# Kernel tuning notes

Measured on AMD Instinct MI355X. Metric: run time of the kernel, lower is better.

Reference implementation:

```python
import jax, jax.numpy as jnp
import numpy as np

ALPHA = 0.2  # LeakyReLU slope
EPS = 1e-5   # LayerNorm eps (torch default)
NEG = -9e15  # pyGAT mask fill


def _lnorm(x, g, b):
    mu = x.mean(-1, keepdims=True)
    var = ((x - mu) ** 2).mean(-1, keepdims=True)
    return (x - mu) / jnp.sqrt(var + EPS) * g + b


def _gat_rel(h, adj, W, a1, a2):
    # Canonical dense GAT layer, vectorized over relations.
    # h [N,di], adj [R,N,N] int, W [R,di,do], a1/a2 [R,do]
    Wh = jnp.einsum('ni,rio->rno', h, W)                     # [R,N,do]
    f1 = jnp.einsum('rno,ro->rn', Wh, a1)
    f2 = jnp.einsum('rno,ro->rn', Wh, a2)
    e = jax.nn.leaky_relu(f1[:, :, None] + f2[:, None, :], ALPHA)  # [R,N,N]
    att = jax.nn.softmax(jnp.where(adj > 0, e, NEG), axis=-1)
    return jax.nn.elu(jnp.einsum('rnm,rmo->rno', att, Wh))   # [R,N,do]


def setup_inputs() -> dict:
    key = jax.random.key(0)
    N, D, R, Q, C = 2048, 512, 4, 32, 64
    HE, HD = 2, 2
    ks = jax.random.split(key, 16)
    s = 0.05
    return {
        'x': jax.random.normal(ks[0], (N, D), jnp.float32),
        'rel_adj': jax.random.randint(ks[1], (R, N, N), 0, 2, jnp.int32),
        'qembedding1': jax.random.normal(ks[2], (Q, D), jnp.float32),
        'qnode_idx': jax.random.randint(ks[3], (8,), 0, N, jnp.int32),
        'choices_nodes_idx': jax.random.randint(ks[4], (5, C), 0, N, jnp.int32),
        'Wc': jax.random.normal(ks[5], (D, D), jnp.float32) * s,
        'bc': jnp.zeros((D,), jnp.float32),
        'wq': jax.random.normal(ks[6], (D,), jnp.float32) * s,
        'enc_W': jax.random.normal(ks[7], (HE, R, D, D), jnp.float32) * s,
        'enc_a1': jax.random.normal(ks[8], (HE, R, D), jnp.float32) * s,
        'enc_a2': jax.random.normal(ks[9], (HE, R, D), jnp.float32) * s,
        'dec_W': jax.random.normal(ks[10], (HD, R, D, D), jnp.float32) * s,
        'dec_a1': jax.random.normal(ks[11], (HD, R, D), jnp.float32) * s,
        'dec_a2': jax.random.normal(ks[12], (HD, R, D), jnp.float32) * s,
        'ln_g': jnp.ones((D,), jnp.float32),
        'ln_b': jnp.zeros((D,), jnp.float32),
        'Wqc': jax.random.normal(ks[13], (D, D), jnp.float32) * s,
        'bqc': jnp.zeros((D,), jnp.float32),
        'Wout': jax.random.normal(ks[14], (D, 1), jnp.float32) * s,
        'bout': jnp.zeros((1,), jnp.float32),
    }


def reference(x, rel_adj, qembedding1, qnode_idx, choices_nodes_idx,
              Wc, bc, wq, enc_W, enc_a1, enc_a2, dec_W, dec_a1, dec_a2,
              ln_g, ln_b, Wqc, bqc, Wout, bout):
    # QuestionLayer: attention-pool the question token sequence -> [D]
    qemb = jax.nn.softmax(qembedding1 @ wq) @ qembedding1
    # question-gated node embeddings (Conv1d k=1 == linear over features)
    p = jax.nn.sigmoid((x @ Wc.T + bc) @ qemb)[:, None]       # [N,1]
    x = p * x + (1.0 - p) * qemb[None, :]
    # encoder: per-relation GAT + LayerNorm, maxpool over relations
    for h in range(enc_W.shape[0]):
        xr = _gat_rel(x, rel_adj, enc_W[h], enc_a1[h], enc_a2[h])
        x = _lnorm(xr, ln_g, ln_b).max(axis=0)                # [N,D]
    # decoder (transpose attentions): last round skips LayerNorm
    xd = x
    HD = dec_W.shape[0]
    for i in range(HD):
        xr = _gat_rel(xd, rel_adj, dec_W[i], dec_a1[i], dec_a2[i])
        if i < HD - 1:
            xr = _lnorm(xr, ln_g, ln_b)
        xd = xr.max(axis=0)
    # QuestionChoiceLayer over the 5 choices (all present -> mask gate = 1)
    cnodes = x[choices_nodes_idx]                             # [5,C,D]
    qproj = qembedding1.mean(axis=0) @ Wqc + bqc              # [D]
    scores = jax.nn.softmax(jnp.einsum('kcd,d->kc', cnodes, qproj), axis=-1)
    cembed = jnp.einsum('kc,kcd->kd', scores, cnodes)         # [5,D]
    cout = jax.nn.log_softmax(cembed @ Wout + bout, axis=0)   # [5,1]
    return cout, xd
```

## Files before the change

kernel.cpp:

```cpp
#include <hip/hip_runtime.h>
#include <hip/hip_bf16.h>

typedef __hip_bfloat16 bf16;
typedef __attribute__((ext_vector_type(8))) short bf16x8_t;
typedef __attribute__((ext_vector_type(4))) float f32x4_t;

#define N 2048
#define D 512
#define R 4
#define Q 32
#define NC 64
#define ALPHA 0.2f
#define LNEPS 1e-5f
#define NEGC -9e15f
#define PLS 44

__device__ __forceinline__ float ldf(const float* p) { return *p; }
__device__ __forceinline__ float ldf(const bf16* p) { return __bfloat162float(*p); }
__device__ __forceinline__ void stf(float* p, float v) { *p = v; }
__device__ __forceinline__ void stf(bf16* p, float v) { *p = __float2bfloat16(v); }

__device__ __forceinline__ short f2b(float f) {
    unsigned u = __builtin_bit_cast(unsigned, f);
    unsigned r = u + 0x7FFFu + ((u >> 16) & 1u);
    return (short)(r >> 16);
}
__device__ __forceinline__ float b2fs(short s) {
    unsigned u = ((unsigned)(unsigned short)s) << 16;
    return __builtin_bit_cast(float, u);
}
__device__ __forceinline__ unsigned pk2(float a, float b) {
    return (unsigned)(unsigned short)f2b(a) | (((unsigned)(unsigned short)f2b(b)) << 16);
}

__device__ __forceinline__ float waveReduceSum(float v) {
#pragma unroll
    for (int o = 32; o > 0; o >>= 1) v += __shfl_down(v, o, 64);
    return v;
}
__device__ __forceinline__ float waveReduceMax(float v) {
#pragma unroll
    for (int o = 32; o > 0; o >>= 1) v = fmaxf(v, __shfl_down(v, o, 64));
    return v;
}

__global__ __launch_bounds__(512) void k_prep(const float* __restrict__ qe1, const float* __restrict__ wq,
                                              const float* __restrict__ Wc, const float* __restrict__ bc,
                                              const float* __restrict__ Wqc, const float* __restrict__ bqc,
                                              float* __restrict__ qemb, float* __restrict__ vvec,
                                              float* __restrict__ qproj, float* __restrict__ c0) {
    __shared__ float logits[Q];
    __shared__ float sw[Q];
    __shared__ float meanq[D];
    __shared__ float qembs[D];
    __shared__ float red8[8];
    int tid = threadIdx.x;
    int wave = tid >> 6, lane = tid & 63;
    for (int q = wave; q < Q; q += 8) {
        float s = 0.f;
        for (int d = lane; d < D; d += 64) s += qe1[q * D + d] * wq[d];
        s = waveReduceSum(s);
        if (lane == 0) logits[q] = s;
    }
    __syncthreads();
    if (tid == 0) {
        float m = -3e38f;
        for (int q = 0; q < Q; q++) m = fmaxf(m, logits[q]);
        float ssum = 0.f;
        for (int q = 0; q < Q; q++) { float e = __expf(logits[q] - m); sw[q] = e; ssum += e; }
        float inv = 1.f / ssum;
        for (int q = 0; q < Q; q++) sw[q] *= inv;
    }
    __syncthreads();
    {
        float acc = 0.f, mq = 0.f;
#pragma unroll 4
        for (int q = 0; q < Q; q++) { float xv = qe1[q * D + tid]; acc += sw[q] * xv; mq += xv; }
        qembs[tid] = acc;
        meanq[tid] = mq * (1.f / Q);
        qemb[tid] = acc;
    }
    __syncthreads();
    {
        float v = 0.f, qp = 0.f;
        for (int i = 0; i < D; i++) {
            v = fmaf(qembs[i], Wc[i * D + tid], v);
            qp = fmaf(meanq[i], Wqc[i * D + tid], qp);
        }
        vvec[tid] = v;
        qproj[tid] = qp + bqc[tid];
    }
    float cc = qembs[tid] * bc[tid];
    cc = waveReduceSum(cc);
    if (lane == 0) red8[wave] = cc;
    __syncthreads();
    if (tid == 0) {
        float t = 0.f;
        for (int i = 0; i < 8; i++) t += red8[i];
        c0[0] = t;
    }
}

__global__ __launch_bounds__(256) void k_prepw(const float* __restrict__ W, short* __restrict__ Wt,
                                               float* __restrict__ f1, float* __restrict__ f2) {
    int mi = blockIdx.z;
    int k0 = blockIdx.y * 32, d0 = blockIdx.x * 32;
    __shared__ float L[32][33];
    int tid = threadIdx.x;
    if (blockIdx.y == 0 && tid < 128) {
        int base = mi * N + blockIdx.x * 128 + tid;
        f1[base] = 0.f;
        f2[base] = 0.f;
    }
    const float* Wm = W + (size_t)mi * D * D;
    {
        int kr = tid >> 3, dc = (tid & 7) * 4;
        float4 f = *(const float4*)&Wm[(size_t)(k0 + kr) * D + d0 + dc];
        L[kr][dc] = f.x; L[kr][dc + 1] = f.y; L[kr][dc + 2] = f.z; L[kr][dc + 3] = f.w;
    }
    __syncthreads();
    short* Wo = Wt + (size_t)mi * D * D;
    {
        int dr = tid >> 3, kc = (tid & 7) * 4;
        uint2 o;
        o.x = pk2(L[kc][dr], L[kc + 1][dr]);
        o.y = pk2(L[kc + 2][dr], L[kc + 3][dr]);
        *(uint2*)&Wo[(size_t)(d0 + dr) * D + k0 + kc] = o;
    }
}

__global__ __launch_bounds__(256) void k_gate(const float* __restrict__ x, const float* __restrict__ vvec,
                                              const float* __restrict__ qemb, const float* __restrict__ c0,
                                              bf16* __restrict__ xcur) {
    int n = blockIdx.x;
    int tid = threadIdx.x;
    __shared__ float red[4];
    __shared__ float ps;
    float x0 = x[n * D + tid], x1 = x[n * D + tid + 256];
    float v = x0 * vvec[tid] + x1 * vvec[tid + 256];
    v = waveReduceSum(v);
    if ((tid & 63) == 0) red[tid >> 6] = v;
    __syncthreads();
    if (tid == 0) {
        float dot = (red[0] + red[1]) + (red[2] + red[3]) + c0[0];
        ps = 1.f / (1.f + __expf(-dot));
    }
    __syncthreads();
    float p = ps;
    stf(&xcur[n * D + tid], p * x0 + (1.f - p) * qemb[tid]);
    stf(&xcur[n * D + tid + 256], p * x1 + (1.f - p) * qemb[tid + 256]);
}

__global__ __launch_bounds__(256) void k_gemm_mfma(const bf16* __restrict__ xin, const short* __restrict__ Wt,
                                                   short* __restrict__ WhT, const float* __restrict__ a1b,
                                                   const float* __restrict__ a2b, float* __restrict__ f1,
                                                   float* __restrict__ f2) {
    int r = blockIdx.z;
    int m0 = blockIdx.x * 64;
    int d0 = blockIdx.y * 64;
    int tid = threadIdx.x;
    int w = tid >> 6, l = tid & 63, g = l >> 4, rs = l & 15;
    int wn = w >> 1, wd = w & 1;
    __shared__ __align__(16) short Al[64 * 40];
    __shared__ __align__(16) short Bl[64 * 40];
    __shared__ __align__(16) short Tt[64 * 80];
    __shared__ float a1s[64], a2s[64];
    __shared__ float r1[4][64], r2[4][64];
    if (tid < 64) {
        a1s[tid] = a1b[r * D + d0 + tid];
        a2s[tid] = a2b[r * D + d0 + tid];
    }
    f32x4_t acc[2][2];
#pragma unroll
    for (int i = 0; i < 2; i++)
#pragma unroll
        for (int j = 0; j < 2; j++) acc[i][j] = (f32x4_t)(0.0f);

    const short* Wtr = Wt + (size_t)r * D * D;
    int sn = tid >> 2;
    int sk = (tid & 3) * 8;
    for (int k0 = 0; k0 < D; k0 += 32) {
        __syncthreads();
        {
            *(uint4*)&Al[sn * 40 + sk] = *(const uint4*)&xin[(size_t)(m0 + sn) * D + k0 + sk];
            *(uint4*)&Bl[sn * 40 + sk] = *(const uint4*)&Wtr[(size_t)(d0 + sn) * D + k0 + sk];
        }
        __syncthreads();
        union UA { bf16x8_t v; uint2 u[2]; };
        UA a[2], b;
#pragma unroll
        for (int nf = 0; nf < 2; nf++) {
            int arow = wn * 32 + nf * 16 + rs;
            a[nf].u[0] = *(const uint2*)&Al[arow * 40 + 4 * g];
            a[nf].u[1] = *(const uint2*)&Al[arow * 40 + 16 + 4 * g];
        }
#pragma unroll
        for (int df = 0; df < 2; df++) {
            int brow = wd * 32 + df * 16 + rs;
            b.u[0] = *(const uint2*)&Bl[brow * 40 + 4 * g];
            b.u[1] = *(const uint2*)&Bl[brow * 40 + 16 + 4 * g];
            acc[0][df] = __builtin_amdgcn_mfma_f32_16x16x32_bf16(a[0].v, b.v, acc[0][df], 0, 0, 0);
            acc[1][df] = __builtin_amdgcn_mfma_f32_16x16x32_bf16(a[1].v, b.v, acc[1][df], 0, 0, 0);
        }
    }
    __syncthreads();
#pragma unroll
    for (int nf = 0; nf < 2; nf++)
#pragma unroll
        for (int df = 0; df < 2; df++) {
            int nl = wn * 32 + nf * 16 + 4 * g;
            int dl = wd * 32 + df * 16 + rs;
            uint2 o;
            o.x = pk2(acc[nf][df][0], acc[nf][df][1]);
            o.y = pk2(acc[nf][df][2], acc[nf][df][3]);
            *(uint2*)&Tt[dl * 80 + nl] = o;
        }
    __syncthreads();
    {
        int dl = tid >> 2;
        int nc = (tid & 3) * 16;
        uint4 v0 = *(const uint4*)&Tt[dl * 80 + nc];
        uint4 v1 = *(const uint4*)&Tt[dl * 80 + nc + 8];
        short* op = WhT + ((size_t)r * D + d0 + dl) * N + m0 + nc;
        *(uint4*)op = v0;
        *(uint4*)(op + 8) = v1;
    }
    {
        int m = tid & 63, dg = tid >> 6;
        float s1 = 0.f, s2 = 0.f;
#pragma unroll
        for (int d = 0; d < 16; d++) {
            int dd = dg + d * 4;
            float wv = b2fs(Tt[dd * 80 + m]);
            s1 = fmaf(wv, a1s[dd], s1);
            s2 = fmaf(wv, a2s[dd], s2);
        }
        r1[dg][m] = s1;
        r2[dg][m] = s2;
    }
    __syncthreads();
    if (tid < 64) {
        float v1 = (r1[0][tid] + r1[1][tid]) + (r1[2][tid] + r1[3][tid]);
        float v2 = (r2[0][tid] + r2[1][tid]) + (r2[2][tid] + r2[3][tid]);
        atomicAdd(&f1[r * N + m0 + tid], v1);
        atomicAdd(&f2[r * N + m0 + tid], v2);
    }
}

__global__ __launch_bounds__(512, 2) void k_pv_nm(const int* __restrict__ adj, const float* __restrict__ f1,
                                                  const float* __restrict__ f2, const short* __restrict__ WhT,
                                                  bf16* __restrict__ xr) {
    int r = blockIdx.y;
    int n0 = blockIdx.x * 32;
    int tid = threadIdx.x;
    int w = tid >> 6, l = tid & 63, g = l >> 4, rs = l & 15;
    __shared__ __align__(16) short Pl[2][32 * PLS];
    __shared__ __align__(16) short Whl[2][512 * PLS];
    __shared__ float sl[32], f1s[32];
    if (tid < 32) f1s[tid] = f1[r * N + n0 + tid];
    __syncthreads();
    f32x4_t acc[2][4];
#pragma unroll
    for (int i = 0; i < 2; i++)
#pragma unroll
        for (int j = 0; j < 4; j++) acc[i][j] = (f32x4_t)(0.0f);

    int pn = tid >> 3, pm4 = (tid & 7) * 4;
    const float* f2r = f2 + r * N;
    const int* arowb = adj + ((size_t)r * N + n0 + (pn & 31)) * N + pm4;
    int4 avA, avB;
    float4 fvA, fvB;
    float f1v = 0.f;
    float myl = 0.f;
    int j = tid - 256;
    uint4 wreg[8];
    if (tid < 256) {
        f1v = f1s[pn];
        avA = *(const int4*)(arowb);
        fvA = *(const float4*)&f2r[pm4];
        avB = *(const int4*)(arowb + 32);
        fvB = *(const float4*)&f2r[32 + pm4];
    } else {
#pragma unroll
        for (int i = 0; i < 8; i++) {
            int v = j + i * 256;
            int dd = v >> 2, mc = (v & 3) * 8;
            wreg[i] = *(const uint4*)&WhT[((size_t)r * D + dd) * N + mc];
        }
    }

    const int NT = N / 32;

#define PRODUCE(tt, cc, AV, FV)                                                                      \
    if (tid < 256) {                                                                                 \
        float t0 = f1v + FV.x; t0 = t0 >= 0.f ? t0 : ALPHA * t0;                                     \
        float t1 = f1v + FV.y; t1 = t1 >= 0.f ? t1 : ALPHA * t1;                                     \
        float t2 = f1v + FV.z; t2 = t2 >= 0.f ? t2 : ALPHA * t2;                                     \
        float t3 = f1v + FV.w; t3 = t3 >= 0.f ? t3 : ALPHA * t3;                                     \
        float e0 = (AV.x > 0) ? __expf(fminf(t0, 60.f)) : 0.f;                                       \
        float e1 = (AV.y > 0) ? __expf(fminf(t1, 60.f)) : 0.f;                                       \
        float e2 = (AV.z > 0) ? __expf(fminf(t2, 60.f)) : 0.f;                                       \
        float e3 = (AV.w > 0) ? __expf(fminf(t3, 60.f)) : 0.f;                                       \
        myl += (e0 + e1) + (e2 + e3);                                                                \
        uint2 pw;                                                                                    \
        pw.x = pk2(e0, e1);                                                                          \
        pw.y = pk2(e2, e3);                                                                          \
        *(uint2*)&Pl[cc][pn * PLS + pm4] = pw;                                                       \
        if ((tt) + 2 < NT) {                                                                         \
            AV = *(const int4*)(arowb + ((tt) + 2) * 32);                                            \
            FV = *(const float4*)&f2r[((tt) + 2) * 32 + pm4];                                        \
        }                                                                                            \
    } else {                                                                                         \
        _Pragma("unroll") for (int i = 0; i < 8; i++) {                                              \
            int v = j + i * 256;                                                                     \
            int dd = v >> 2, mc = (v & 3) * 8;                                                       \
            uint2 lo; lo.x = wreg[i].x; lo.y = wreg[i].y;                                            \
            uint2 hi; hi.x = wreg[i].z; hi.y = wreg[i].w;                                            \
            *(uint2*)&Whl[cc][dd * PLS + mc] = lo;                                                   \
            *(uint2*)&Whl[cc][dd * PLS + mc + 4] = hi;                                               \
        }                                                                                            \
        if ((tt) + 1 < NT) {                                                                         \
            _Pragma("unroll") for (int i = 0; i < 8; i++) {                                          \
                int v = j + i * 256;                                                                 \
                int dd = v >> 2, mc = (v & 3) * 8;                                                   \
                wreg[i] = *(const uint4*)&WhT[((size_t)r * D + dd) * N + ((tt) + 1) * 32 + mc];      \
            }                                                                                        \
        }                                                                                            \
    }

#define MFMASTEP(cc)                                                                                 \
    {                                                                                                \
        union UA { bf16x8_t v; uint2 u[2]; };                                                        \
        UA a[2], bb;                                                                                 \
        _Pragma("unroll") for (int nf = 0; nf < 2; nf++) {                                           \
            int arow = nf * 16 + rs;                                                                 \
            a[nf].u[0] = *(const uint2*)&Pl[cc][arow * PLS + 4 * g];                                 \
            a[nf].u[1] = *(const uint2*)&Pl[cc][arow * PLS + 16 + 4 * g];                            \
        }                                                                                            \
        _Pragma("unroll") for (int df = 0; df < 4; df++) {                                           \
            int brow = w * 64 + df * 16 + rs;                                                        \
            bb.u[0] = *(const uint2*)&Whl[cc][brow * PLS + 4 * g];                                   \
            bb.u[1] = *(const uint2*)&Whl[cc][brow * PLS + 16 + 4 * g];                              \
            acc[0][df] = __builtin_amdgcn_mfma_f32_16x16x32_bf16(a[0].v, bb.v, acc[0][df], 0, 0, 0); \
            acc[1][df] = __builtin_amdgcn_mfma_f32_16x16x32_bf16(a[1].v, bb.v, acc[1][df], 0, 0, 0); \
        }                                                                                            \
    }

    PRODUCE(0, 0, avA, fvA);
    __syncthreads();
    for (int t = 0; t < NT; t += 2) {
        if (t + 1 < NT) { PRODUCE(t + 1, 1, avB, fvB); }
        MFMASTEP(0);
        __syncthreads();
        if (t + 2 < NT) { PRODUCE(t + 2, 0, avA, fvA); }
        MFMASTEP(1);
        __syncthreads();
    }
#undef PRODUCE
#undef MFMASTEP
    if (tid < 256) {
        float v = myl;
#pragma unroll
        for (int msk = 1; msk < 8; msk <<= 1) v += __shfl_xor(v, msk, 8);
        if ((tid & 7) == 0) sl[pn] = v;
    }
    __syncthreads();
    float inv[2][4];
#pragma unroll
    for (int nf = 0; nf < 2; nf++)
#pragma unroll
        for (int reg = 0; reg < 4; reg++) inv[nf][reg] = 1.f / sl[nf * 16 + 4 * g + reg];
#pragma unroll
    for (int nf = 0; nf < 2; nf++)
#pragma unroll
        for (int df = 0; df < 4; df++)
#pragma unroll
            for (int reg = 0; reg < 4; reg++) {
                int n = n0 + nf * 16 + 4 * g + reg;
                int d = w * 64 + df * 16 + rs;
                float v = acc[nf][df][reg] * inv[nf][reg];
                v = v > 0.f ? v : (__expf(v) - 1.f);
                stf(&xr[((size_t)r * N + n) * D + d], v);
            }
}

__global__ __launch_bounds__(256) void k_lnmax(const bf16* __restrict__ xr, const float* __restrict__ g,
                                               const float* __restrict__ b, bf16* __restrict__ xout) {
    int n = blockIdx.x;
    int tid = threadIdx.x;
    int wave = tid >> 6, lane = tid & 63;
    __shared__ float redA[4], redB[4];
    float g0 = g[tid], g1 = g[tid + 256];
    float bb0 = b[tid], bb1 = b[tid + 256];
    float mx0 = -3e38f, mx1 = -3e38f;
    for (int r = 0; r < R; r++) {
        const bf16* row = xr + ((size_t)(r * N + n)) * D;
        float v0 = ldf(&row[tid]), v1 = ldf(&row[tid + 256]);
        float s = v0 + v1;
        float ss = fmaf(v0, v0, v1 * v1);
        s = waveReduceSum(s);
        ss = waveReduceSum(ss);
        if (lane == 0) { redA[wave] = s; redB[wave] = ss; }
        __syncthreads();
        float mu = ((redA[0] + redA[1]) + (redA[2] + redA[3])) * (1.f / D);
        float ex2 = ((redB[0] + redB[1]) + (redB[2] + redB[3])) * (1.f / D);
        float inv = 1.f / sqrtf(ex2 - mu * mu + LNEPS);
        mx0 = fmaxf(mx0, (v0 - mu) * inv * g0 + bb0);
        mx1 = fmaxf(mx1, (v1 - mu) * inv * g1 + bb1);
        __syncthreads();
    }
    stf(&xout[n * D + tid], mx0);
    stf(&xout[n * D + tid + 256], mx1);
}

__global__ __launch_bounds__(256) void k_maxout(const bf16* __restrict__ xr, float* __restrict__ out) {
    size_t idx = (size_t)blockIdx.x * 256 + threadIdx.x;
    float m = ldf(&xr[idx]);
    m = fmaxf(m, ldf(&xr[(size_t)N * D + idx]));
    m = fmaxf(m, ldf(&xr[2 * (size_t)N * D + idx]));
    m = fmaxf(m, ldf(&xr[3 * (size_t)N * D + idx]));
    out[idx] = m;
}

__global__ __launch_bounds__(256) void k_cscore(const bf16* __restrict__ xe, const int* __restrict__ cidx,
                                                const float* __restrict__ qproj, const float* __restrict__ Wout,
                                                float* __restrict__ scw, float* __restrict__ dvw) {
    int wv = threadIdx.x >> 6, lane = threadIdx.x & 63;
    int p = blockIdx.x * 4 + wv;
    const bf16* row = xe + (size_t)cidx[p] * D;
    float s1 = 0.f, s2 = 0.f;
#pragma unroll
    for (int i = 0; i < 8; i++) {
        int d = lane + i * 64;
        float v = ldf(&row[d]);
        s1 = fmaf(v, qproj[d], s1);
        s2 = fmaf(v, Wout[d], s2);
    }
    s1 = waveReduceSum(s1);
    s2 = waveReduceSum(s2);
    if (lane == 0) { scw[p] = s1; dvw[p] = s2; }
}

__global__ __launch_bounds__(64) void k_cfinal(const float* __restrict__ scw, const float* __restrict__ dvw,
                                               const float* __restrict__ bout, float* __restrict__ out) {
    int lane = threadIdx.x;
    __shared__ float lg[5];
    for (int k = 0; k < 5; k++) {
        float v = scw[k * NC + lane];
        float m = waveReduceMax(v);
        m = __shfl(m, 0, 64);
        float e = __expf(v - m);
        float s = waveReduceSum(e);
        s = __shfl(s, 0, 64);
        float t = (e / s) * dvw[k * NC + lane];
        t = waveReduceSum(t);
        if (lane == 0) lg[k] = t + bout[0];
    }
    __syncthreads();
    if (lane == 0) {
        float m = -3e38f;
        for (int k = 0; k < 5; k++) m = fmaxf(m, lg[k]);
        float s = 0.f;
        for (int k = 0; k < 5; k++) s += __expf(lg[k] - m);
        float lse = logf(s) + m;
        for (int k = 0; k < 5; k++) out[k] = lg[k] - lse;
    }
}

extern "C" void kernel_launch(void* const* d_in, const int* in_sizes, int n_in,
                              void* d_out, int out_size, void* d_ws, size_t ws_size,
                              hipStream_t stream) {
    bool skipQ = false;
    if (n_in > 4 && in_sizes[4] != 5 * NC && in_sizes[3] == 5 * NC) skipQ = true;
    auto IN = [&](int i) -> const void* {
        int j = (skipQ && i >= 4) ? i - 1 : i;
        return d_in[j];
    };
    const float* x = (const float*)IN(0);
    const int* adj = (const int*)IN(1);
    const float* qe1 = (const float*)IN(2);
    const int* cidx = (const int*)IN(4);
    const float* Wc = (const float*)IN(5);
    const float* bc = (const float*)IN(6);
    const float* wq = (const float*)IN(7);
    const float* encW = (const float*)IN(8);
    const float* enca1 = (const float*)IN(9);
    const float* enca2 = (const float*)IN(10);
    const float* decW = (const float*)IN(11);
    const float* deca1 = (const float*)IN(12);
    const float* deca2 = (const float*)IN(13);
    const float* lng = (const float*)IN(14);
    const float* lnb = (const float*)IN(15);
    const float* Wqc = (const float*)IN(16);
    const float* bqc = (const float*)IN(17);
    const float* Wout = (const float*)IN(18);
    const float* bout = (const float*)IN(19);
    float* out = (float*)d_out;

    char* w8 = (char*)d_ws;
    float* qemb = (float*)(w8 + 0);
    float* vvec = (float*)(w8 + 2048);
    float* qproj = (float*)(w8 + 4096);
    float* c0 = (float*)(w8 + 6144);
    float* f1 = (float*)(w8 + 8192);
    float* f2 = (float*)(w8 + 8192 + 32768);
    float* scw = (float*)(w8 + 8192 + 65536);
    float* dvw = (float*)(w8 + 8192 + 98304);
    const size_t ND = (size_t)N * D;
    bf16* xcur = (bf16*)(w8 + 139264);
    bf16* xd = (bf16*)(w8 + 139264 + ND * 2);
    short* WhT = (short*)(w8 + 139264 + ND * 4);
    bf16* xr = (bf16*)(w8 + 139264 + ND * 4 + R * ND * 2);
    short* Wt = (short*)xr;

    k_prep<<<1, 512, 0, stream>>>(qe1, wq, Wc, bc, Wqc, bqc, qemb, vvec, qproj, c0);
    k_gate<<<N, 256, 0, stream>>>(x, vvec, qemb, c0, xcur);

    for (int L = 0; L < 4; L++) {
        const float* Wb = (L < 2) ? encW + (size_t)L * R * D * D : decW + (size_t)(L - 2) * R * D * D;
        const float* a1 = (L < 2) ? enca1 + L * R * D : deca1 + (L - 2) * R * D;
        const float* a2 = (L < 2) ? enca2 + L * R * D : deca2 + (L - 2) * R * D;
        const bf16* xin = (L == 3) ? xd : xcur;
        k_prepw<<<dim3(16, 16, R), 256, 0, stream>>>(Wb, Wt, f1, f2);
        k_gemm_mfma<<<dim3(N / 64, D / 64, R), 256, 0, stream>>>(xin, Wt, WhT, a1, a2, f1, f2);
        k_pv_nm<<<dim3(N / 32, R), 512, 0, stream>>>(adj, f1, f2, WhT, xr);
        if (L < 3)
            k_lnmax<<<N, 256, 0, stream>>>(xr, lng, lnb, (L < 2) ? xcur : xd);
        else
            k_maxout<<<N * D / 256, 256, 0, stream>>>(xr, out + 5);
    }
    k_cscore<<<80, 256, 0, stream>>>(xcur, cidx, qproj, Wout, scw, dvw);
    k_cfinal<<<1, 64, 0, stream>>>(scw, dvw, bout, out);
}
```

Measured before the change: 367.5 us.

## Load Wh B-fragments directly from global into registers, spread P production over all threads

The PV kernel no longer stages the transposed Wh tile through shared memory. Each wave now loads its MFMA B-fragments straight from global memory into double-buffered registers. P-tile production (exp of masked scores) is spread across all 512 threads at two elements each, replacing the previous split between producer and copier thread halves. This frees a large amount of LDS, which may raise occupancy, and removes LDS write/read traffic. The cost is uncoalesced 8-byte global loads, and Wh is no longer shared across waves through LDS, so L2 traffic goes up.

```diff
diff --git a/kernel.cpp b/kernel.cpp
--- a/kernel.cpp
+++ b/kernel.cpp
@@ -255,7 +255,6 @@
     int tid = threadIdx.x;
     int w = tid >> 6, l = tid & 63, g = l >> 4, rs = l & 15;
     __shared__ __align__(16) short Pl[2][32 * PLS];
-    __shared__ __align__(16) short Whl[2][512 * PLS];
     __shared__ float sl[32], f1s[32];
     if (tid < 32) f1s[tid] = f1[r * N + n0 + tid];
     __syncthreads();
@@ -265,70 +264,45 @@
 #pragma unroll
         for (int j = 0; j < 4; j++) acc[i][j] = (f32x4_t)(0.0f);
 
-    int pn = tid >> 3, pm4 = (tid & 7) * 4;
+    int pn = tid >> 4, pm2 = (tid & 15) * 2;
     const float* f2r = f2 + r * N;
-    const int* arowb = adj + ((size_t)r * N + n0 + (pn & 31)) * N + pm4;
-    int4 avA, avB;
-    float4 fvA, fvB;
-    float f1v = 0.f;
+    const int* arowb = adj + ((size_t)r * N + n0 + pn) * N + pm2;
+    float f1v = f1s[pn];
     float myl = 0.f;
-    int j = tid - 256;
-    uint4 wreg[8];
-    if (tid < 256) {
-        f1v = f1s[pn];
-        avA = *(const int4*)(arowb);
-        fvA = *(const float4*)&f2r[pm4];
-        avB = *(const int4*)(arowb + 32);
-        fvB = *(const float4*)&f2r[32 + pm4];
-    } else {
-#pragma unroll
-        for (int i = 0; i < 8; i++) {
-            int v = j + i * 256;
-            int dd = v >> 2, mc = (v & 3) * 8;
-            wreg[i] = *(const uint4*)&WhT[((size_t)r * D + dd) * N + mc];
-        }
-    }
+
+    const short* bp[4];
+#pragma unroll
+    for (int df = 0; df < 4; df++)
+        bp[df] = WhT + ((size_t)r * D + w * 64 + df * 16 + rs) * N + 4 * g;
+
+    uint2 bregA[8], bregB[8];
+    int2 avA, avB;
+    float2 fvA, fvB;
 
     const int NT = N / 32;
 
-#define PRODUCE(tt, cc, AV, FV)                                                                      \
-    if (tid < 256) {                                                                                 \
-        float t0 = f1v + FV.x; t0 = t0 >= 0.f ? t0 : ALPHA * t0;                                     \
-        float t1 = f1v + FV.y; t1 = t1 >= 0.f ? t1 : ALPHA * t1;                                     \
-        float t2 = f1v + FV.z; t2 = t2 >= 0.f ? t2 : ALPHA * t2;                                     \
-        float t3 = f1v + FV.w; t3 = t3 >= 0.f ? t3 : ALPHA * t3;                                     \
-        float e0 = (AV.x > 0) ? __expf(fminf(t0, 60.f)) : 0.f;                                       \
-        float e1 = (AV.y > 0) ? __expf(fminf(t1, 60.f)) : 0.f;                                       \
-        float e2 = (AV.z > 0) ? __expf(fminf(t2, 60.f)) : 0.f;                                       \
-        float e3 = (AV.w > 0) ? __expf(fminf(t3, 60.f)) : 0.f;                                       \
-        myl += (e0 + e1) + (e2 + e3);                                                                \
-        uint2 pw;                                                                                    \
-        pw.x = pk2(e0, e1);                                                                          \
-        pw.y = pk2(e2, e3);                                                                          \
-        *(uint2*)&Pl[cc][pn * PLS + pm4] = pw;                                                       \
-        if ((tt) + 2 < NT) {                                                                         \
-            AV = *(const int4*)(arowb + ((tt) + 2) * 32);                                            \
-            FV = *(const float4*)&f2r[((tt) + 2) * 32 + pm4];                                        \
-        }                                                                                            \
-    } else {                                                                                         \
-        _Pragma("unroll") for (int i = 0; i < 8; i++) {                                              \
-            int v = j + i * 256;                                                                     \
-            int dd = v >> 2, mc = (v & 3) * 8;                                                       \
-            uint2 lo; lo.x = wreg[i].x; lo.y = wreg[i].y;                                            \
-            uint2 hi; hi.x = wreg[i].z; hi.y = wreg[i].w;                                            \
-            *(uint2*)&Whl[cc][dd * PLS + mc] = lo;                                                   \
-            *(uint2*)&Whl[cc][dd * PLS + mc + 4] = hi;                                               \
-        }                                                                                            \
-        if ((tt) + 1 < NT) {                                                                         \
-            _Pragma("unroll") for (int i = 0; i < 8; i++) {                                          \
-                int v = j + i * 256;                                                                 \
-                int dd = v >> 2, mc = (v & 3) * 8;                                                   \
-                wreg[i] = *(const uint4*)&WhT[((size_t)r * D + dd) * N + ((tt) + 1) * 32 + mc];      \
-            }                                                                                        \
-        }                                                                                            \
-    }
-
-#define MFMASTEP(cc)                                                                                 \
+#define LOADB(BR, tt)                                                   \
+    _Pragma("unroll") for (int df = 0; df < 4; df++) {                  \
+        const short* p = bp[df] + (tt) * 32;                            \
+        BR[2 * df] = *(const uint2*)p;                                  \
+        BR[2 * df + 1] = *(const uint2*)(p + 16);                       \
+    }
+
+#define PROD(tt, cc, AV, FV)                                            \
+    {                                                                   \
+        float t0 = f1v + FV.x; t0 = t0 >= 0.f ? t0 : ALPHA * t0;        \
+        float t1 = f1v + FV.y; t1 = t1 >= 0.f ? t1 : ALPHA * t1;        \
+        float e0 = (AV.x > 0) ? __expf(fminf(t0, 60.f)) : 0.f;          \
+        float e1 = (AV.y > 0) ? __expf(fminf(t1, 60.f)) : 0.f;          \
+        myl += e0 + e1;                                                 \
+        *(unsigned*)&Pl[cc][pn * PLS + pm2] = pk2(e0, e1);              \
+        if ((tt) + 2 < NT) {                                            \
+            AV = *(const int2*)(arowb + ((tt) + 2) * 32);               \
+            FV = *(const float2*)&f2r[((tt) + 2) * 32 + pm2];           \
+        }                                                               \
+    }
+
+#define MFMASTEP(cc, BR)                                                                             \
     {                                                                                                \
         union UA { bf16x8_t v; uint2 u[2]; };                                                        \
         UA a[2], bb;                                                                                 \
@@ -338,31 +312,36 @@
             a[nf].u[1] = *(const uint2*)&Pl[cc][arow * PLS + 16 + 4 * g];                            \
         }                                                                                            \
         _Pragma("unroll") for (int df = 0; df < 4; df++) {                                           \
-            int brow = w * 64 + df * 16 + rs;                                                        \
-            bb.u[0] = *(const uint2*)&Whl[cc][brow * PLS + 4 * g];                                   \
-            bb.u[1] = *(const uint2*)&Whl[cc][brow * PLS + 16 + 4 * g];                              \
+            bb.u[0] = BR[2 * df];                                                                    \
+            bb.u[1] = BR[2 * df + 1];                                                                \
             acc[0][df] = __builtin_amdgcn_mfma_f32_16x16x32_bf16(a[0].v, bb.v, acc[0][df], 0, 0, 0); \
             acc[1][df] = __builtin_amdgcn_mfma_f32_16x16x32_bf16(a[1].v, bb.v, acc[1][df], 0, 0, 0); \
         }                                                                                            \
     }
 
-    PRODUCE(0, 0, avA, fvA);
+    avA = *(const int2*)arowb;
+    fvA = *(const float2*)&f2r[pm2];
+    avB = *(const int2*)(arowb + 32);
+    fvB = *(const float2*)&f2r[32 + pm2];
+    LOADB(bregA, 0);
+    PROD(0, 0, avA, fvA);
     __syncthreads();
     for (int t = 0; t < NT; t += 2) {
-        if (t + 1 < NT) { PRODUCE(t + 1, 1, avB, fvB); }
-        MFMASTEP(0);
+        if (t + 1 < NT) { PROD(t + 1, 1, avB, fvB); LOADB(bregB, t + 1); }
+        MFMASTEP(0, bregA);
         __syncthreads();
-        if (t + 2 < NT) { PRODUCE(t + 2, 0, avA, fvA); }
-        MFMASTEP(1);
+        if (t + 2 < NT) { PROD(t + 2, 0, avA, fvA); LOADB(bregA, t + 2); }
+        MFMASTEP(1, bregB);
         __syncthreads();
     }
-#undef PRODUCE
+#undef LOADB
+#undef PROD
 #undef MFMASTEP
-    if (tid < 256) {
+    {
         float v = myl;
 #pragma unroll
-        for (int msk = 1; msk < 8; msk <<= 1) v += __shfl_xor(v, msk, 8);
-        if ((tid & 7) == 0) sl[pn] = v;
+        for (int msk = 1; msk < 16; msk <<= 1) v += __shfl_xor(v, msk, 16);
+        if ((tid & 15) == 0) sl[pn] = v;
     }
     __syncthreads();
     float inv[2][4];
```

After: 665.3 us. 1.81x slower.
